# Kernel optimization log

Measured on AMD Instinct MI355X. Metric: run time of the kernel, lower is better.

Reference implementation:

```python
import jax, jax.numpy as jnp
import numpy as np

EPS = 1e-12  # torch F.normalize eps
K = 32       # num_clusters (hardcoded in module)

def l2norm(v, axis):
    n = jnp.sqrt(jnp.sum(v * v, axis=axis, keepdims=True))
    return v / jnp.maximum(n, EPS)

def setup_inputs() -> dict:
    key = jax.random.key(0)
    k1, k2, k3, k4 = jax.random.split(key, 4)
    B, M, D = 64, 128, 2048
    x = jax.random.normal(k1, (B, M, D), dtype=jnp.float32)
    # ragged lengths in [1, M]
    lengths = jax.random.randint(k2, (B,), 0, M, dtype=jnp.int32) + 1
    init_sc = 1.0 / np.sqrt(D)
    W = init_sc * jax.random.normal(k3, (K, D), dtype=jnp.float32)  # fc1.weight
    C = init_sc * jax.random.normal(k4, (K, D), dtype=jnp.float32)  # centroids
    return {"x": x, "lengths": lengths, "W": W, "C": C}

def reference(x, lengths, W, C):
    # x: [B,M,D] padded frames, lengths: [B] valid frame counts
    B, M, D = x.shape
    mask = (jnp.arange(M)[None, :] < lengths[:, None]).astype(x.dtype)  # [B,M]
    cnt = lengths.astype(x.dtype)[:, None]                              # [B,1]
    # avg pooling over valid (raw, un-normalized) frames
    avgpool = jnp.sum(x * mask[:, :, None], axis=1) / cnt               # [B,D]
    # per-frame L2 normalize
    xn = l2norm(x, axis=-1)                                             # [B,M,D]
    # soft assignment: linear (no bias) + softmax over clusters
    logits = jnp.einsum('bmd,kd->bmk', xn, W)
    a = jax.nn.softmax(logits, axis=-1) * mask[:, :, None]              # [B,M,K]
    # VLAD residual aggregation, GEMM form:
    # sum_m a[b,m,k]*(xn[b,m,:] - C[k,:]) = (a^T xn) - C * sum_m a
    ax = jnp.einsum('bmk,bmd->bkd', a, xn)                              # [B,K,D]
    asum = jnp.sum(a, axis=1)                                           # [B,K]
    vlad = ax - asum[:, :, None] * C[None, :, :]                        # [B,K,D]
    # intra-normalize per cluster, flatten, global L2 normalize
    vlad = l2norm(vlad, axis=2)
    vlad = vlad.reshape(B, K * D)
    vlad = l2norm(vlad, axis=1)
    return jnp.concatenate([avgpool, vlad], axis=1)                     # [B, D + K*D]
```

## Files before the change

kernel.cpp:

```cpp
#include <hip/hip_runtime.h>
#include <math.h>

#define BB 64
#define MM 128
#define DDIM 2048
#define KK 32
#define NFR (BB*MM)
#define OUTROW (DDIM + KK*DDIM)

typedef __attribute__((ext_vector_type(8))) short bf16x8;
typedef __attribute__((ext_vector_type(4))) float f32x4;

__device__ __forceinline__ short f2bf(float f) {
  unsigned u = __builtin_bit_cast(unsigned, f);
  u += 0x7fffu + ((u >> 16) & 1u);
  return (short)(u >> 16);
}

__global__ __launch_bounds__(256) void k_prep(const float* __restrict__ W,
                                              short* __restrict__ Wb) {
  int i = (blockIdx.x * 256 + threadIdx.x) * 8;
  float4 a = *(const float4*)(W + i);
  float4 b = *(const float4*)(W + i + 4);
  bf16x8 o = {f2bf(a.x), f2bf(a.y), f2bf(a.z), f2bf(a.w),
              f2bf(b.x), f2bf(b.y), f2bf(b.z), f2bf(b.w)};
  *(bf16x8*)(Wb + i) = o;
}

__global__ __launch_bounds__(256) void k_logits(const float* __restrict__ x,
    const int* __restrict__ lengths, const short* __restrict__ Wb,
    short* __restrict__ aT, float* __restrict__ asum) {
  const int t = threadIdx.x, wv = t >> 6, lane = t & 63;
  const int l15 = lane & 15, quad = lane >> 4;
  const int fg = blockIdx.x;
  const int g0 = fg * 16;
  const int b  = fg >> 3;
  const int m0 = (fg & 7) * 16;
  const int len = lengths[b];

  const float* xrow = x + (size_t)(g0 + l15) * DDIM + wv * 512 + quad * 8;
  const short* w0   = Wb + l15 * DDIM + wv * 512 + quad * 8;
  const short* w1   = w0 + 16 * DDIM;

  f32x4 c0 = {0.f, 0.f, 0.f, 0.f}, c1 = {0.f, 0.f, 0.f, 0.f};
  float ssq = 0.f;
  #pragma unroll
  for (int s = 0; s < 16; ++s) {
    float4 xa = *(const float4*)(xrow + s * 32);
    float4 xc = *(const float4*)(xrow + s * 32 + 4);
    ssq = fmaf(xa.x, xa.x, ssq); ssq = fmaf(xa.y, xa.y, ssq);
    ssq = fmaf(xa.z, xa.z, ssq); ssq = fmaf(xa.w, xa.w, ssq);
    ssq = fmaf(xc.x, xc.x, ssq); ssq = fmaf(xc.y, xc.y, ssq);
    ssq = fmaf(xc.z, xc.z, ssq); ssq = fmaf(xc.w, xc.w, ssq);
    bf16x8 A = {f2bf(xa.x), f2bf(xa.y), f2bf(xa.z), f2bf(xa.w),
                f2bf(xc.x), f2bf(xc.y), f2bf(xc.z), f2bf(xc.w)};
    bf16x8 B0 = *(const bf16x8*)(w0 + s * 32);
    bf16x8 B1 = *(const bf16x8*)(w1 + s * 32);
    c0 = __builtin_amdgcn_mfma_f32_16x16x32_bf16(A, B0, c0, 0, 0, 0);
    c1 = __builtin_amdgcn_mfma_f32_16x16x32_bf16(A, B1, c1, 0, 0, 0);
  }

  ssq += __shfl_xor(ssq, 16, 64);
  ssq += __shfl_xor(ssq, 32, 64);
  __shared__ float sq[4][16];
  __shared__ float lg[4][16][33];
  if (quad == 0) sq[wv][l15] = ssq;
  #pragma unroll
  for (int r = 0; r < 4; ++r) {
    lg[wv][quad * 4 + r][l15]      = c0[r];
    lg[wv][quad * 4 + r][16 + l15] = c1[r];
  }
  __syncthreads();

  const int fr = t >> 4, kk = (t & 15) * 2;
  float s0 = 0.f, s1 = 0.f;
  #pragma unroll
  for (int w = 0; w < 4; ++w) { s0 += lg[w][fr][kk]; s1 += lg[w][fr][kk + 1]; }
  float ss  = sq[0][fr] + sq[1][fr] + sq[2][fr] + sq[3][fr];
  float inv = 1.f / fmaxf(sqrtf(ss), 1e-12f);
  s0 *= inv; s1 *= inv;
  float mx = fmaxf(s0, s1);
  mx = fmaxf(mx, __shfl_xor(mx, 1, 64));
  mx = fmaxf(mx, __shfl_xor(mx, 2, 64));
  mx = fmaxf(mx, __shfl_xor(mx, 4, 64));
  mx = fmaxf(mx, __shfl_xor(mx, 8, 64));
  float e0 = __expf(s0 - mx), e1 = __expf(s1 - mx);
  float se = e0 + e1;
  se += __shfl_xor(se, 1, 64);
  se += __shfl_xor(se, 2, 64);
  se += __shfl_xor(se, 4, 64);
  se += __shfl_xor(se, 8, 64);
  const bool valid = (m0 + fr) < len;
  float rr = valid ? (1.f / se) : 0.f;
  float a0 = e0 * rr, a1 = e1 * rr;

  __syncthreads();
  lg[0][fr][kk] = a0; lg[0][fr][kk + 1] = a1;
  __syncthreads();
  if (t < KK) {
    float s = 0.f;
    #pragma unroll
    for (int f = 0; f < 16; ++f) s += lg[0][f][t];
    atomicAdd(asum + b * KK + t, s);
  }
  short* ap = aT + (size_t)b * KK * MM + m0 + fr;
  ap[(size_t)kk * MM]       = f2bf(a0 * inv);
  ap[(size_t)(kk + 1) * MM] = f2bf(a1 * inv);
}

__global__ __launch_bounds__(256) void k_vlad(const float* __restrict__ x,
    const int* __restrict__ lengths, const float* __restrict__ Cc,
    const short* __restrict__ aT, const float* __restrict__ asum,
    float* __restrict__ out, float* __restrict__ ssq_part) {
  const int t = threadIdx.x, wv = t >> 6, lane = t & 63;
  const int l15 = lane & 15, quad = lane >> 4;
  const int dc = blockIdx.x, b = blockIdx.y;
  const int d0 = dc * 256 + wv * 64;
  const int len = lengths[b];
  const float* xb = x + (size_t)b * MM * DDIM;
  const short* at0 = aT + (size_t)b * KK * MM + l15 * MM + quad * 8;

  f32x4 acc[2][4];
  #pragma unroll
  for (int kt = 0; kt < 2; ++kt)
    #pragma unroll
    for (int nt = 0; nt < 4; ++nt) acc[kt][nt] = (f32x4){0.f, 0.f, 0.f, 0.f};
  float avg[4] = {0.f, 0.f, 0.f, 0.f};

  #pragma unroll
  for (int ms = 0; ms < 4; ++ms) {
    const int m0 = ms * 32;
    bf16x8 A0 = *(const bf16x8*)(at0 + m0);
    bf16x8 A1 = *(const bf16x8*)(at0 + 16 * MM + m0);
    #pragma unroll
    for (int nt = 0; nt < 4; ++nt) {
      const float* xc = xb + (size_t)(m0 + quad * 8) * DDIM + d0 + nt * 16 + l15;
      float xv[8];
      #pragma unroll
      for (int j = 0; j < 8; ++j) xv[j] = xc[(size_t)j * DDIM];
      #pragma unroll
      for (int j = 0; j < 8; ++j)
        avg[nt] += (m0 + quad * 8 + j < len) ? xv[j] : 0.f;
      bf16x8 B = {f2bf(xv[0]), f2bf(xv[1]), f2bf(xv[2]), f2bf(xv[3]),
                  f2bf(xv[4]), f2bf(xv[5]), f2bf(xv[6]), f2bf(xv[7])};
      acc[0][nt] = __builtin_amdgcn_mfma_f32_16x16x32_bf16(A0, B, acc[0][nt], 0, 0, 0);
      acc[1][nt] = __builtin_amdgcn_mfma_f32_16x16x32_bf16(A1, B, acc[1][nt], 0, 0, 0);
    }
  }

  #pragma unroll
  for (int nt = 0; nt < 4; ++nt) {
    float a = avg[nt];
    a += __shfl_xor(a, 16, 64);
    a += __shfl_xor(a, 32, 64);
    if (quad == 0) out[(size_t)b * OUTROW + d0 + nt * 16 + l15] = a / (float)len;
  }

  __shared__ float ssw[4][33];
  float* orow = out + (size_t)b * OUTROW + DDIM;
  #pragma unroll
  for (int kt = 0; kt < 2; ++kt) {
    #pragma unroll
    for (int r = 0; r < 4; ++r) {
      const int k = kt * 16 + quad * 4 + r;
      const float as = asum[b * KK + k];
      float sqv = 0.f;
      #pragma unroll
      for (int nt = 0; nt < 4; ++nt) {
        const int d = d0 + nt * 16 + l15;
        float v = acc[kt][nt][r] - as * Cc[(size_t)k * DDIM + d];
        orow[(size_t)k * DDIM + d] = v;
        sqv = fmaf(v, v, sqv);
      }
      sqv += __shfl_xor(sqv, 1, 64);
      sqv += __shfl_xor(sqv, 2, 64);
      sqv += __shfl_xor(sqv, 4, 64);
      sqv += __shfl_xor(sqv, 8, 64);
      if (l15 == 0) ssw[wv][k] = sqv;
    }
  }
  __syncthreads();
  if (t < KK)
    ssq_part[((size_t)dc * BB + b) * KK + t] =
        ssw[0][t] + ssw[1][t] + ssw[2][t] + ssw[3][t];
}

__global__ __launch_bounds__(256) void k_norm(const float* __restrict__ ssq_part,
    float* __restrict__ out) {
  const int t = threadIdx.x;
  const int k = blockIdx.x;
  const int b = blockIdx.y;
  __shared__ float ssk[32];
  if (t < 32) {
    float sk = 0.f;
    #pragma unroll
    for (int dc = 0; dc < 8; ++dc)
      sk += ssq_part[((size_t)dc * BB + b) * KK + t];
    ssk[t] = sk;
  }
  __syncthreads();
  float gss = 0.f, iv_own = 0.f;
  #pragma unroll
  for (int kk = 0; kk < 32; ++kk) {
    float nk = sqrtf(ssk[kk]);
    float iv = 1.f / fmaxf(nk, 1e-12f);
    float nn = nk * iv;
    gss += nn * nn;
    if (kk == k) iv_own = iv;
  }
  float sc = iv_own / fmaxf(sqrtf(gss), 1e-12f);
  float* row = out + (size_t)b * OUTROW + DDIM + (size_t)k * DDIM;
  #pragma unroll
  for (int h = 0; h < 2; ++h) {
    float4* p = (float4*)(row + h * 1024 + t * 4);
    float4 v = *p;
    v.x *= sc; v.y *= sc; v.z *= sc; v.w *= sc;
    *p = v;
  }
}

extern "C" void kernel_launch(void* const* d_in, const int* in_sizes, int n_in,
                              void* d_out, int out_size, void* d_ws, size_t ws_size,
                              hipStream_t stream) {
  const float* x       = (const float*)d_in[0];
  const int*   lengths = (const int*)d_in[1];
  const float* W       = (const float*)d_in[2];
  const float* C       = (const float*)d_in[3];
  float* out = (float*)d_out;

  short* Wb   = (short*)d_ws;
  short* aT   = Wb + (size_t)KK * DDIM;
  float* asum = (float*)(aT + (size_t)BB * KK * MM);
  float* ssqp = asum + (size_t)BB * KK;

  hipMemsetAsync(asum, 0, (size_t)BB * KK * sizeof(float), stream);
  k_prep  <<<dim3(32),      256, 0, stream>>>(W, Wb);
  k_logits<<<dim3(512),     256, 0, stream>>>(x, lengths, Wb, aT, asum);
  k_vlad  <<<dim3(8, BB),   256, 0, stream>>>(x, lengths, C, aT, asum, out, ssqp);
  k_norm  <<<dim3(KK, BB),  256, 0, stream>>>(ssqp, out);
}
```

Baseline: 148.2 us.

## Stage x tile through LDS transpose in k_vlad and replace asum atomics with partials

k_vlad now loads x with coalesced float4 row reads, converts to bf16 and writes a transposed tile into shared memory, then reads MFMA B operands from LDS. Previously each lane did eight strided scalar global loads. The atomicAdd accumulation of asum is replaced by per-block partial sums that k_vlad reduces itself, which also removes the memset launch. This adds LDS traffic and a block sync, and keeps the ms loop rolled.

```diff
diff --git a/kernel.cpp b/kernel.cpp
--- a/kernel.cpp
+++ b/kernel.cpp
@@ -15,6 +15,9 @@
   unsigned u = __builtin_bit_cast(unsigned, f);
   u += 0x7fffu + ((u >> 16) & 1u);
   return (short)(u >> 16);
+}
+__device__ __forceinline__ unsigned pack2(float lo, float hi) {
+  return (unsigned)(unsigned short)f2bf(lo) | ((unsigned)(unsigned short)f2bf(hi) << 16);
 }
 
 __global__ __launch_bounds__(256) void k_prep(const float* __restrict__ W,
@@ -29,7 +32,7 @@
 
 __global__ __launch_bounds__(256) void k_logits(const float* __restrict__ x,
     const int* __restrict__ lengths, const short* __restrict__ Wb,
-    short* __restrict__ aT, float* __restrict__ asum) {
+    short* __restrict__ aT, float* __restrict__ asum_p) {
   const int t = threadIdx.x, wv = t >> 6, lane = t & 63;
   const int l15 = lane & 15, quad = lane >> 4;
   const int fg = blockIdx.x;
@@ -101,7 +104,7 @@
     float s = 0.f;
     #pragma unroll
     for (int f = 0; f < 16; ++f) s += lg[0][f][t];
-    atomicAdd(asum + b * KK + t, s);
+    asum_p[(size_t)fg * KK + t] = s;
   }
   short* ap = aT + (size_t)b * KK * MM + m0 + fr;
   ap[(size_t)kk * MM]       = f2bf(a0 * inv);
@@ -110,14 +113,26 @@
 
 __global__ __launch_bounds__(256) void k_vlad(const float* __restrict__ x,
     const int* __restrict__ lengths, const float* __restrict__ Cc,
-    const short* __restrict__ aT, const float* __restrict__ asum,
+    const short* __restrict__ aT, const float* __restrict__ asum_p,
     float* __restrict__ out, float* __restrict__ ssq_part) {
   const int t = threadIdx.x, wv = t >> 6, lane = t & 63;
   const int l15 = lane & 15, quad = lane >> 4;
   const int dc = blockIdx.x, b = blockIdx.y;
-  const int d0 = dc * 256 + wv * 64;
+  const int dw0 = dc * 256 + wv * 64;
   const int len = lengths[b];
-  const float* xb = x + (size_t)b * MM * DDIM;
+
+  __shared__ short xbt[4][64][40];
+  __shared__ float asl[KK];
+  __shared__ float ssw[4][33];
+
+  if (t < KK) {
+    float s = 0.f;
+    #pragma unroll
+    for (int p = 0; p < 8; ++p) s += asum_p[(size_t)(b * 8 + p) * KK + t];
+    asl[t] = s;
+  }
+
+  const float* xb  = x  + (size_t)b * MM * DDIM;
   const short* at0 = aT + (size_t)b * KK * MM + l15 * MM + quad * 8;
 
   f32x4 acc[2][4];
@@ -127,47 +142,62 @@
     for (int nt = 0; nt < 4; ++nt) acc[kt][nt] = (f32x4){0.f, 0.f, 0.f, 0.f};
   float avg[4] = {0.f, 0.f, 0.f, 0.f};
 
-  #pragma unroll
+  const int q4   = l15 * 4;
+  const int mrow = (lane >> 4) * 2;
+
   for (int ms = 0; ms < 4; ++ms) {
     const int m0 = ms * 32;
+    #pragma unroll
+    for (int p = 0; p < 4; ++p) {
+      int ml = p * 8 + mrow;
+      int m  = m0 + ml;
+      const float* xr = xb + (size_t)m * DDIM + dw0 + q4;
+      float4 v0 = *(const float4*)xr;
+      float4 v1 = *(const float4*)(xr + DDIM);
+      float f0 = (m < len) ? 1.f : 0.f;
+      float f1 = (m + 1 < len) ? 1.f : 0.f;
+      avg[0] = fmaf(v0.x, f0, fmaf(v1.x, f1, avg[0]));
+      avg[1] = fmaf(v0.y, f0, fmaf(v1.y, f1, avg[1]));
+      avg[2] = fmaf(v0.z, f0, fmaf(v1.z, f1, avg[2]));
+      avg[3] = fmaf(v0.w, f0, fmaf(v1.w, f1, avg[3]));
+      *(unsigned*)&xbt[wv][q4 + 0][ml] = pack2(v0.x, v1.x);
+      *(unsigned*)&xbt[wv][q4 + 1][ml] = pack2(v0.y, v1.y);
+      *(unsigned*)&xbt[wv][q4 + 2][ml] = pack2(v0.z, v1.z);
+      *(unsigned*)&xbt[wv][q4 + 3][ml] = pack2(v0.w, v1.w);
+    }
     bf16x8 A0 = *(const bf16x8*)(at0 + m0);
     bf16x8 A1 = *(const bf16x8*)(at0 + 16 * MM + m0);
     #pragma unroll
     for (int nt = 0; nt < 4; ++nt) {
-      const float* xc = xb + (size_t)(m0 + quad * 8) * DDIM + d0 + nt * 16 + l15;
-      float xv[8];
-      #pragma unroll
-      for (int j = 0; j < 8; ++j) xv[j] = xc[(size_t)j * DDIM];
-      #pragma unroll
-      for (int j = 0; j < 8; ++j)
-        avg[nt] += (m0 + quad * 8 + j < len) ? xv[j] : 0.f;
-      bf16x8 B = {f2bf(xv[0]), f2bf(xv[1]), f2bf(xv[2]), f2bf(xv[3]),
-                  f2bf(xv[4]), f2bf(xv[5]), f2bf(xv[6]), f2bf(xv[7])};
+      bf16x8 B = *(const bf16x8*)&xbt[wv][nt * 16 + l15][quad * 8];
       acc[0][nt] = __builtin_amdgcn_mfma_f32_16x16x32_bf16(A0, B, acc[0][nt], 0, 0, 0);
       acc[1][nt] = __builtin_amdgcn_mfma_f32_16x16x32_bf16(A1, B, acc[1][nt], 0, 0, 0);
     }
   }
 
   #pragma unroll
-  for (int nt = 0; nt < 4; ++nt) {
-    float a = avg[nt];
-    a += __shfl_xor(a, 16, 64);
-    a += __shfl_xor(a, 32, 64);
-    if (quad == 0) out[(size_t)b * OUTROW + d0 + nt * 16 + l15] = a / (float)len;
-  }
-
-  __shared__ float ssw[4][33];
+  for (int c = 0; c < 4; ++c) {
+    avg[c] += __shfl_xor(avg[c], 16, 64);
+    avg[c] += __shfl_xor(avg[c], 32, 64);
+  }
+  if (quad == 0) {
+    float rl = 1.f / (float)len;
+    *(float4*)(out + (size_t)b * OUTROW + dw0 + q4) =
+        make_float4(avg[0] * rl, avg[1] * rl, avg[2] * rl, avg[3] * rl);
+  }
+
+  __syncthreads();
   float* orow = out + (size_t)b * OUTROW + DDIM;
   #pragma unroll
   for (int kt = 0; kt < 2; ++kt) {
     #pragma unroll
     for (int r = 0; r < 4; ++r) {
       const int k = kt * 16 + quad * 4 + r;
-      const float as = asum[b * KK + k];
+      const float as = asl[k];
       float sqv = 0.f;
       #pragma unroll
       for (int nt = 0; nt < 4; ++nt) {
-        const int d = d0 + nt * 16 + l15;
+        const int d = dw0 + nt * 16 + l15;
         float v = acc[kt][nt][r] - as * Cc[(size_t)k * DDIM + d];
         orow[(size_t)k * DDIM + d] = v;
         sqv = fmaf(v, v, sqv);
@@ -228,14 +258,13 @@
   const float* C       = (const float*)d_in[3];
   float* out = (float*)d_out;
 
-  short* Wb   = (short*)d_ws;
-  short* aT   = Wb + (size_t)KK * DDIM;
-  float* asum = (float*)(aT + (size_t)BB * KK * MM);
-  float* ssqp = asum + (size_t)BB * KK;
-
-  hipMemsetAsync(asum, 0, (size_t)BB * KK * sizeof(float), stream);
-  k_prep  <<<dim3(32),      256, 0, stream>>>(W, Wb);
-  k_logits<<<dim3(512),     256, 0, stream>>>(x, lengths, Wb, aT, asum);
-  k_vlad  <<<dim3(8, BB),   256, 0, stream>>>(x, lengths, C, aT, asum, out, ssqp);
-  k_norm  <<<dim3(KK, BB),  256, 0, stream>>>(ssqp, out);
-}
+  short* Wb     = (short*)d_ws;
+  short* aT     = Wb + (size_t)KK * DDIM;
+  float* asum_p = (float*)(aT + (size_t)BB * KK * MM);
+  float* ssqp   = asum_p + (size_t)512 * KK;
+
+  k_prep  <<<dim3(32),     256, 0, stream>>>(W, Wb);
+  k_logits<<<dim3(512),    256, 0, stream>>>(x, lengths, Wb, aT, asum_p);
+  k_vlad  <<<dim3(8, BB),  256, 0, stream>>>(x, lengths, C, aT, asum_p, out, ssqp);
+  k_norm  <<<dim3(KK, BB), 256, 0, stream>>>(ssqp, out);
+}
```

New measurement: 146.1 us. No clear change (-1.4%).
